# Optimization experiments

Measured on AMD Instinct MI355X. Metric: run time of the kernel, lower is better.

The kernel has to match this reference:

```python
import jax, jax.numpy as jnp
import numpy as np

D_MODEL = 512
NUM_HEADS = 8
D_K = D_MODEL // NUM_HEADS
LN_EPS = 1e-5


def setup_inputs() -> dict:
    key = jax.random.key(0)
    ks = jax.random.split(key, 11)
    d = D_MODEL
    s = 1.0 / np.sqrt(d)
    return {
        "x": jax.random.normal(ks[0], (4, 2048, d), dtype=jnp.float32),
        "Wq": jax.random.uniform(ks[1], (d, d), jnp.float32, -s, s),
        "bq": jax.random.uniform(ks[2], (d,), jnp.float32, -s, s),
        "Wk": jax.random.uniform(ks[3], (d, d), jnp.float32, -s, s),
        "bk": jax.random.uniform(ks[4], (d,), jnp.float32, -s, s),
        "Wv": jax.random.uniform(ks[5], (d, d), jnp.float32, -s, s),
        "bv": jax.random.uniform(ks[6], (d,), jnp.float32, -s, s),
        "Wo": jax.random.uniform(ks[7], (d, d), jnp.float32, -s, s),
        "bo": jax.random.uniform(ks[8], (d,), jnp.float32, -s, s),
        "gamma": jnp.ones((d,), jnp.float32),
        "beta": jnp.zeros((d,), jnp.float32),
    }


def reference(x, Wq, bq, Wk, bk, Wv, bv, Wo, bo, gamma, beta):
    # x: (B, S, D). Dropout is identity (eval mode).
    B, S, D = x.shape
    H, dk = NUM_HEADS, D_K
    # Linear layers use torch convention: y = x @ W.T + b
    q = (x @ Wq.T + bq).reshape(B, S, H, dk).transpose(0, 2, 1, 3)  # (B,H,S,dk)
    k = (x @ Wk.T + bk).reshape(B, S, H, dk).transpose(0, 2, 1, 3)
    v = (x @ Wv.T + bv).reshape(B, S, H, dk).transpose(0, 2, 1, 3)
    scores = jnp.einsum("bhqd,bhkd->bhqk", q, k) / jnp.sqrt(jnp.float32(dk))
    attn = jax.nn.softmax(scores, axis=-1)
    ctx = jnp.einsum("bhqk,bhkd->bhqd", attn, v)  # (B,H,S,dk)
    ctx = ctx.transpose(0, 2, 1, 3).reshape(B, S, D)
    out = ctx @ Wo.T + bo
    # residual + LayerNorm
    y = x + out
    mu = jnp.mean(y, axis=-1, keepdims=True)
    var = jnp.mean(jnp.square(y - mu), axis=-1, keepdims=True)
    return (y - mu) / jnp.sqrt(var + LN_EPS) * gamma + beta
```

## Files before the change

kernel.cpp:

```cpp
#include <hip/hip_runtime.h>
#include <math.h>

#define D 512
#define NH 8
#define DK 64
#define S 2048
#define BATCH 4
#define N_TOK (BATCH * S)

#define QSCALE 0.18033688f

typedef __bf16 bf16x8 __attribute__((ext_vector_type(8)));
typedef __bf16 bf16x4 __attribute__((ext_vector_type(4)));
typedef float f32x4 __attribute__((ext_vector_type(4)));

#define AS1 __attribute__((address_space(1)))
#define AS3 __attribute__((address_space(3)))

#define OFF_XB   0
#define OFF_WB   8388608
#define OFF_Q    10485760
#define OFF_K    18874368
#define OFF_VT   27262976
#define OFF_CTX  35651584
#define OFF_Y    10485760
#define OFF_FLAG 44040192

static __device__ __forceinline__ bf16x8 ldg8(const __bf16* p) {
    return *(const bf16x8*)p;
}
static __device__ __forceinline__ f32x4 mfma16(bf16x8 a, bf16x8 b, f32x4 c) {
    return __builtin_amdgcn_mfma_f32_16x16x32_bf16(a, b, c, 0, 0, 0);
}
static __device__ __forceinline__ float ldf(const void* p, size_t i, int isf) {
    return isf ? ((const float*)p)[i] : (float)(((const __bf16*)p)[i]);
}
static __device__ __forceinline__ float fexp2(float x) {
#if __has_builtin(__builtin_amdgcn_exp2f)
    return __builtin_amdgcn_exp2f(x);
#else
    return exp2f(x);
#endif
}
static __device__ __forceinline__ unsigned pack_trunc(float e0, float e1) {
    return (__builtin_bit_cast(unsigned, e0) >> 16)
         | (__builtin_bit_cast(unsigned, e1) & 0xFFFF0000u);
}
static __device__ __forceinline__ void gload_lds16(const void* g, void* l) {
    __builtin_amdgcn_global_load_lds((const AS1 char*)g, (AS3 char*)l, 16, 0, 0);
}

__global__ __launch_bounds__(256)
void cvt_kernel(const void* __restrict__ x,  const void* __restrict__ Wq,
                const void* __restrict__ Wk, const void* __restrict__ Wv,
                const void* __restrict__ Wo, __bf16* __restrict__ xb,
                __bf16* __restrict__ Wb, int* __restrict__ flag)
{
    const bf16x8 probe = ldg8((const __bf16*)x + (threadIdx.x & 63) * 8);
    int bad = 0;
#pragma unroll
    for (int j = 0; j < 8; ++j) bad |= !(fabsf((float)probe[j]) <= 64.0f);
    const int isf = __any(bad) ? 1 : 0;
    if (blockIdx.x == 0 && threadIdx.x == 0) *flag = isf;

    const size_t i0 = ((size_t)blockIdx.x * 256 + threadIdx.x) * 8;
    const void* src;
    __bf16* dst;
    size_t off;
    if (i0 < 4194304) {
        src = x; off = i0; dst = xb + i0;
    } else {
        const size_t wrel = i0 - 4194304;
        const size_t w = wrel >> 18;
        src = (w == 0) ? Wq : (w == 1) ? Wk : (w == 2) ? Wv : Wo;
        off = wrel & 262143;
        dst = Wb + wrel;
    }
    bf16x8 r;
    if (isf) {
        const float* f = (const float*)src + off;
#pragma unroll
        for (int j = 0; j < 8; ++j) r[j] = (__bf16)f[j];
    } else {
        r = *(const bf16x8*)((const __bf16*)src + off);
    }
    *(bf16x8*)dst = r;
}

__global__ __launch_bounds__(256)
void qkv_kernel(const __bf16* __restrict__ xb, const __bf16* __restrict__ Wb,
                const void* __restrict__ bq, const void* __restrict__ bk,
                const void* __restrict__ bv, const int* __restrict__ flag,
                __bf16* __restrict__ Q, __bf16* __restrict__ K,
                __bf16* __restrict__ Vt)
{
    __shared__ __align__(16) char smem[32768];

    const int isf = *flag;
    const int tid = threadIdx.x;
    const int w = tid >> 6, l = tid & 63;
    const int lane16 = l & 15, quad = l >> 4;
    const int wm = w >> 1, wn = w & 1;
    const int m0 = blockIdx.x * 128;
    const int by = blockIdx.y;
    const int n0 = by * 128;

    const int cwl = w * 64 + l;
    const int g0 = (cwl & 3) ^ ((cwl >> 3) & 3);
    const __bf16* aS0 = xb + (size_t)(m0 + (cwl >> 2)) * D + g0 * 8;
    const __bf16* aS1 = aS0 + (size_t)64 * D;
    const __bf16* bS0 = Wb + (size_t)(n0 + (cwl >> 2)) * D + g0 * 8;
    const __bf16* bS1 = bS0 + (size_t)64 * D;

    const int sw = (quad ^ ((lane16 >> 1) & 3)) * 16;
    const int aoff = (wm * 64 + lane16) * 64 + sw;
    const int boff = 8192 + (wn * 64 + lane16) * 64 + sw;

    f32x4 acc[4][4];
#pragma unroll
    for (int i = 0; i < 4; ++i)
#pragma unroll
        for (int j = 0; j < 4; ++j) acc[i][j] = (f32x4){0,0,0,0};

    gload_lds16(aS0, smem + w * 1024);
    gload_lds16(aS1, smem + 4096 + w * 1024);
    gload_lds16(bS0, smem + 8192 + w * 1024);
    gload_lds16(bS1, smem + 12288 + w * 1024);

    for (int kt = 0; kt < D / 32; ++kt) {
        __syncthreads();

        const char* bufp = smem + (kt & 1) * 16384;
        if (kt + 1 < D / 32) {
            char* nb = smem + ((kt + 1) & 1) * 16384;
            gload_lds16(aS0 + (kt + 1) * 32, nb + w * 1024);
            gload_lds16(aS1 + (kt + 1) * 32, nb + 4096 + w * 1024);
            gload_lds16(bS0 + (kt + 1) * 32, nb + 8192 + w * 1024);
            gload_lds16(bS1 + (kt + 1) * 32, nb + 12288 + w * 1024);
        }

        bf16x8 af[4], bf[4];
#pragma unroll
        for (int i = 0; i < 4; ++i) af[i] = *(const bf16x8*)(bufp + aoff + i * 1024);
#pragma unroll
        for (int j = 0; j < 4; ++j) bf[j] = *(const bf16x8*)(bufp + boff + j * 1024);
#pragma unroll
        for (int i = 0; i < 4; ++i)
#pragma unroll
            for (int j = 0; j < 4; ++j)
                acc[i][j] = mfma16(af[i], bf[j], acc[i][j]);
    }

    const int which = by >> 2;
    const int h = (by * 2 + wn) & 7;
    const float qs = (which == 0) ? QSCALE : 1.0f;
    const void* bias = (which == 0) ? bq : (which == 1) ? bk : bv;
    float bvv[4];
#pragma unroll
    for (int j = 0; j < 4; ++j)
        bvv[j] = ldf(bias, ((by & 3) * 128 + wn * 64 + 16 * j + lane16) & 511, isf);

    const int bb = m0 >> 11;
    const int ssb = (m0 & (S - 1)) + wm * 64;

    if (which < 2) {
        __bf16* out = ((which == 0) ? Q : K) + ((size_t)(bb * NH + h) * S) * DK;
#pragma unroll
        for (int i = 0; i < 4; ++i)
#pragma unroll
            for (int r = 0; r < 4; ++r) {
                const int ss = ssb + i * 16 + quad * 4 + r;
#pragma unroll
                for (int j = 0; j < 4; ++j)
                    out[(size_t)ss * DK + 16 * j + lane16] =
                        (__bf16)((acc[i][j][r] + bvv[j]) * qs);
            }
    } else {
#pragma unroll
        for (int i = 0; i < 4; ++i)
#pragma unroll
            for (int j = 0; j < 4; ++j) {
                const int dkc = 16 * j + lane16;
                __bf16* vp = Vt + ((size_t)(bb * NH + h) * DK + dkc) * S
                                + ssb + i * 16 + quad * 4;
                bf16x4 pkt;
#pragma unroll
                for (int r = 0; r < 4; ++r) pkt[r] = (__bf16)(acc[i][j][r] + bvv[j]);
                *(bf16x4*)vp = pkt;
            }
    }
}

__global__ __launch_bounds__(256)
void attn_kernel(const __bf16* __restrict__ Q, const __bf16* __restrict__ K,
                 const __bf16* __restrict__ Vt, __bf16* __restrict__ ctx)
{
    __shared__ __align__(16) char smem[49152];

    const int tid = threadIdx.x;
    const int w = tid >> 6, l = tid & 63;
    const int lane16 = l & 15, quad = l >> 4;

    const int lin = blockIdx.x;
    const int xcd = lin & 7;
    const int t = lin >> 3;
    const int bh = xcd * 4 + (t >> 4);
    const int qt = t & 15;
    const int b = bh >> 3, h = bh & 7;
    const size_t bhS = (size_t)bh * S;

    const int cwl = w * 64 + l;
    const char* kS[2];
    const char* vS[2];
#pragma unroll
    for (int c = 0; c < 2; ++c) {
        const int s = c * 256 + cwl;
        const int row = s >> 3;
        const int g = (s & 7) ^ (row & 7);
        kS[c] = (const char*)(K + (bhS + row) * DK) + g * 16;
        vS[c] = (const char*)(Vt + ((size_t)bh * DK + row) * S) + g * 16;
    }

    const int qbase = qt * 128 + w * 32;
    bf16x8 qa[2][2];
#pragma unroll
    for (int u = 0; u < 2; ++u) {
        const __bf16* Qp = Q + (bhS + qbase + u * 16 + lane16) * DK + quad * 8;
        qa[u][0] = ldg8(Qp);
        qa[u][1] = ldg8(Qp + 32);
    }

    bf16x8 aones;
#pragma unroll
    for (int j = 0; j < 8; ++j) aones[j] = (__bf16)1.0f;

    const int x7 = lane16 & 7;
    char* pw = smem + 32768 + w * 4096;
    const int pwoff = lane16 * 128 + ((quad & 1) * 8);
    const int proff = lane16 * 128;

    f32x4 o[2][4], lacc[2];
#pragma unroll
    for (int u = 0; u < 2; ++u) {
        lacc[u] = (f32x4){0,0,0,0};
#pragma unroll
        for (int tt = 0; tt < 4; ++tt) o[u][tt] = (f32x4){0,0,0,0};
    }

    gload_lds16(kS[0], smem + w * 1024);
    gload_lds16(kS[1], smem + 4096 + w * 1024);
    gload_lds16(vS[0], smem + 8192 + w * 1024);
    gload_lds16(vS[1], smem + 12288 + w * 1024);

    for (int kc = 0; kc < S / 64; ++kc) {
        __syncthreads();

        const int buf = kc & 1;
        const char* kb = smem + buf * 16384;
        const char* vb = kb + 8192;

        if (kc + 1 < S / 64) {
            char* kb2 = smem + (buf ^ 1) * 16384;
            gload_lds16(kS[0] + (size_t)(kc + 1) * 8192, kb2 + w * 1024);
            gload_lds16(kS[1] + (size_t)(kc + 1) * 8192, kb2 + 4096 + w * 1024);
            gload_lds16(vS[0] + (size_t)(kc + 1) * 128, kb2 + 8192 + w * 1024);
            gload_lds16(vS[1] + (size_t)(kc + 1) * 128, kb2 + 12288 + w * 1024);
        }

        bf16x8 kfA[4], kfB[4];
#pragma unroll
        for (int tt = 0; tt < 4; ++tt) {
            const int base = (tt * 16 + lane16) * 128;
            kfA[tt] = *(const bf16x8*)(kb + base + ((quad ^ x7) * 16));
            kfB[tt] = *(const bf16x8*)(kb + base + (((quad + 4) ^ x7) * 16));
        }

#pragma unroll
        for (int u = 0; u < 2; ++u) {
            f32x4 st[4];
#pragma unroll
            for (int tt = 0; tt < 4; ++tt) {
                f32x4 z = {0,0,0,0};
                z = mfma16(kfA[tt], qa[u][0], z);
                st[tt] = mfma16(kfB[tt], qa[u][1], z);
            }
#pragma unroll
            for (int tt = 0; tt < 4; ++tt) {
                uint2 pkt;
                pkt.x = pack_trunc(fexp2(st[tt][0]), fexp2(st[tt][1]));
                pkt.y = pack_trunc(fexp2(st[tt][2]), fexp2(st[tt][3]));
                *(uint2*)(pw + u * 2048 + pwoff
                          + (((tt * 2 + (quad >> 1)) ^ x7) * 16)) = pkt;
            }
        }

        bf16x8 vA[4], vB[4];
#pragma unroll
        for (int tt = 0; tt < 4; ++tt) {
            const int base = (tt * 16 + lane16) * 128;
            vA[tt] = *(const bf16x8*)(vb + base + ((quad ^ x7) * 16));
            vB[tt] = *(const bf16x8*)(vb + base + (((quad + 4) ^ x7) * 16));
        }
#pragma unroll
        for (int u = 0; u < 2; ++u) {
            const bf16x8 bp0 = *(const bf16x8*)(pw + u * 2048 + proff
                                                + (((0 + quad) ^ x7) * 16));
            const bf16x8 bp1 = *(const bf16x8*)(pw + u * 2048 + proff
                                                + (((4 + quad) ^ x7) * 16));
            lacc[u] = mfma16(aones, bp0, lacc[u]);
            lacc[u] = mfma16(aones, bp1, lacc[u]);
#pragma unroll
            for (int tt = 0; tt < 4; ++tt) {
                o[u][tt] = mfma16(vA[tt], bp0, o[u][tt]);
                o[u][tt] = mfma16(vB[tt], bp1, o[u][tt]);
            }
        }
    }

#pragma unroll
    for (int u = 0; u < 2; ++u) {
        const float inv = 1.0f / lacc[u][0];
        __bf16* cp = ctx + ((size_t)(b * S + qbase + u * 16 + lane16)) * D
                     + h * DK;
#pragma unroll
        for (int tt = 0; tt < 4; ++tt) {
            bf16x4 pkt;
#pragma unroll
            for (int r = 0; r < 4; ++r) pkt[r] = (__bf16)(o[u][tt][r] * inv);
            *(bf16x4*)(cp + tt * 16 + quad * 4) = pkt;
        }
    }
}

__global__ __launch_bounds__(256)
void proj_kernel(const __bf16* __restrict__ ctx, const __bf16* __restrict__ Wb,
                 const void* __restrict__ bo, const __bf16* __restrict__ xb,
                 const int* __restrict__ flag, __bf16* __restrict__ y)
{
    __shared__ __align__(16) char smem[24576];

    const int isf = *flag;
    const int tid = threadIdx.x;
    const int w = tid >> 6, l = tid & 63;
    const int lane16 = l & 15, quad = l >> 4;
    const int wm = w >> 1, wn = w & 1;
    const int m0 = blockIdx.x * 64;
    const int n0 = blockIdx.y * 128;

    const __bf16* Wo = Wb + (size_t)3 * 262144;
    const int cwl = w * 64 + l;
    const int g0 = (cwl & 3) ^ ((cwl >> 3) & 3);
    const __bf16* aS = ctx + (size_t)(m0 + (cwl >> 2)) * D + g0 * 8;
    const __bf16* bS0 = Wo + (size_t)(n0 + (cwl >> 2)) * D + g0 * 8;
    const __bf16* bS1 = bS0 + (size_t)64 * D;

    const int sw = (quad ^ ((lane16 >> 1) & 3)) * 16;
    const int aoff = (wm * 32 + lane16) * 64 + sw;
    const int boff = 4096 + (wn * 64 + lane16) * 64 + sw;

    f32x4 acc[2][4];
#pragma unroll
    for (int i = 0; i < 2; ++i)
#pragma unroll
        for (int j = 0; j < 4; ++j) acc[i][j] = (f32x4){0,0,0,0};

    gload_lds16(aS, smem + w * 1024);
    gload_lds16(bS0, smem + 4096 + w * 1024);
    gload_lds16(bS1, smem + 8192 + w * 1024);

    for (int kt = 0; kt < D / 32; ++kt) {
        __syncthreads();

        const char* bufp = smem + (kt & 1) * 12288;
        if (kt + 1 < D / 32) {
            char* nb = smem + ((kt + 1) & 1) * 12288;
            gload_lds16(aS + (kt + 1) * 32, nb + w * 1024);
            gload_lds16(bS0 + (kt + 1) * 32, nb + 4096 + w * 1024);
            gload_lds16(bS1 + (kt + 1) * 32, nb + 8192 + w * 1024);
        }

        bf16x8 af[2], bf[4];
#pragma unroll
        for (int i = 0; i < 2; ++i) af[i] = *(const bf16x8*)(bufp + aoff + i * 1024);
#pragma unroll
        for (int j = 0; j < 4; ++j) bf[j] = *(const bf16x8*)(bufp + boff + j * 1024);
#pragma unroll
        for (int i = 0; i < 2; ++i)
#pragma unroll
            for (int j = 0; j < 4; ++j)
                acc[i][j] = mfma16(af[i], bf[j], acc[i][j]);
    }

    float bvv[4];
#pragma unroll
    for (int j = 0; j < 4; ++j)
        bvv[j] = ldf(bo, n0 + wn * 64 + 16 * j + lane16, isf);

#pragma unroll
    for (int i = 0; i < 2; ++i)
#pragma unroll
        for (int r = 0; r < 4; ++r) {
            const int tok = m0 + wm * 32 + i * 16 + quad * 4 + r;
#pragma unroll
            for (int j = 0; j < 4; ++j) {
                const size_t idx = (size_t)tok * D + n0 + wn * 64 + 16 * j + lane16;
                y[idx] = (__bf16)(acc[i][j][r] + bvv[j] + (float)xb[idx]);
            }
        }
}

__global__ __launch_bounds__(256)
void ln_kernel(const __bf16* __restrict__ y, const void* __restrict__ gamma,
               const void* __restrict__ beta, const int* __restrict__ flag,
               void* __restrict__ out)
{
    const int isf = *flag;
    const int l = threadIdx.x & 63;
    const int tok = blockIdx.x * 4 + (threadIdx.x >> 6);
    const bf16x8 vv = ldg8(y + (size_t)tok * D + l * 8);

    float v[8];
    float sum = 0.f, sq = 0.f;
#pragma unroll
    for (int j = 0; j < 8; ++j) {
        v[j] = (float)vv[j];
        sum += v[j];
        sq  += v[j] * v[j];
    }
#pragma unroll
    for (int msk = 1; msk < 64; msk <<= 1) {
        sum += __shfl_xor(sum, msk);
        sq  += __shfl_xor(sq,  msk);
    }
    const float mean = sum * (1.0f / D);
    const float var  = sq * (1.0f / D) - mean * mean;
    const float rstd = rsqrtf(var + 1e-5f);

    const size_t base = (size_t)tok * D + l * 8;
#pragma unroll
    for (int j = 0; j < 8; ++j) {
        const float g  = ldf(gamma, l * 8 + j, isf);
        const float be = ldf(beta,  l * 8 + j, isf);
        const float r  = ((v[j] - mean) * rstd) * g + be;
        if (isf) ((float*)out)[base + j] = r;
        else     ((__bf16*)out)[base + j] = (__bf16)r;
    }
}

extern "C" void kernel_launch(void* const* d_in, const int* in_sizes, int n_in,
                              void* d_out, int out_size, void* d_ws,
                              size_t ws_size, hipStream_t stream)
{
    const void* x     = d_in[0];
    const void* Wq    = d_in[1];
    const void* bq    = d_in[2];
    const void* Wk    = d_in[3];
    const void* bk    = d_in[4];
    const void* Wv    = d_in[5];
    const void* bv    = d_in[6];
    const void* Wo    = d_in[7];
    const void* bo    = d_in[8];
    const void* gamma = d_in[9];
    const void* beta  = d_in[10];

    char* ws = (char*)d_ws;
    __bf16* xb  = (__bf16*)(ws + OFF_XB);
    __bf16* Wb  = (__bf16*)(ws + OFF_WB);
    __bf16* Qb  = (__bf16*)(ws + OFF_Q);
    __bf16* Kb  = (__bf16*)(ws + OFF_K);
    __bf16* Vtb = (__bf16*)(ws + OFF_VT);
    __bf16* ctx = (__bf16*)(ws + OFF_CTX);
    __bf16* y   = (__bf16*)(ws + OFF_Y);
    int*    flag = (int*)(ws + OFF_FLAG);

    cvt_kernel<<<5242880 / (256 * 8), 256, 0, stream>>>(
        x, Wq, Wk, Wv, Wo, xb, Wb, flag);
    qkv_kernel<<<dim3(N_TOK / 128, 12), 256, 0, stream>>>(
        xb, Wb, bq, bk, bv, flag, Qb, Kb, Vtb);
    attn_kernel<<<dim3(512), 256, 0, stream>>>(Qb, Kb, Vtb, ctx);
    proj_kernel<<<dim3(N_TOK / 64, 4), 256, 0, stream>>>(
        ctx, Wb, bo, xb, flag, y);
    ln_kernel<<<dim3(N_TOK / 4), 256, 0, stream>>>(y, gamma, beta, flag, d_out);
}
```

Before: 190.5 us.

## Split attention block across 8 waves with 16 query rows each

The attention kernel now launches 512 threads per block instead of 256, and each of the 8 waves handles 16 query rows instead of 32. Each thread loads one K and one V segment per tile instead of two, and the per-wave P scratch shrinks to 2 KB. The goal is to cut per-thread register use and raise the number of waves hiding latency. The cost is that each K/V fragment read from LDS is reused for fewer queries, so LDS traffic per MFMA doubles.

```diff
diff --git a/kernel.cpp b/kernel.cpp
--- a/kernel.cpp
+++ b/kernel.cpp
@@ -191,7 +191,7 @@
     }
 }
 
-__global__ __launch_bounds__(256)
+__global__ __launch_bounds__(512, 4)
 void attn_kernel(const __bf16* __restrict__ Q, const __bf16* __restrict__ K,
                  const __bf16* __restrict__ Vt, __bf16* __restrict__ ctx)
 {
@@ -210,24 +210,17 @@
     const size_t bhS = (size_t)bh * S;
 
     const int cwl = w * 64 + l;
-    const char* kS[2];
-    const char* vS[2];
-#pragma unroll
-    for (int c = 0; c < 2; ++c) {
-        const int s = c * 256 + cwl;
-        const int row = s >> 3;
-        const int g = (s & 7) ^ (row & 7);
-        kS[c] = (const char*)(K + (bhS + row) * DK) + g * 16;
-        vS[c] = (const char*)(Vt + ((size_t)bh * DK + row) * S) + g * 16;
-    }
-
-    const int qbase = qt * 128 + w * 32;
-    bf16x8 qa[2][2];
-#pragma unroll
-    for (int u = 0; u < 2; ++u) {
-        const __bf16* Qp = Q + (bhS + qbase + u * 16 + lane16) * DK + quad * 8;
-        qa[u][0] = ldg8(Qp);
-        qa[u][1] = ldg8(Qp + 32);
+    const int row = cwl >> 3;
+    const int g = (cwl & 7) ^ (row & 7);
+    const char* kS = (const char*)(K + (bhS + row) * DK) + g * 16;
+    const char* vS = (const char*)(Vt + ((size_t)bh * DK + row) * S) + g * 16;
+
+    const int qbase = qt * 128 + w * 16;
+    bf16x8 qa0, qa1;
+    {
+        const __bf16* Qp = Q + (bhS + qbase + lane16) * DK + quad * 8;
+        qa0 = ldg8(Qp);
+        qa1 = ldg8(Qp + 32);
     }
 
     bf16x8 aones;
@@ -235,22 +228,17 @@
     for (int j = 0; j < 8; ++j) aones[j] = (__bf16)1.0f;
 
     const int x7 = lane16 & 7;
-    char* pw = smem + 32768 + w * 4096;
+    char* pw = smem + 32768 + w * 2048;
     const int pwoff = lane16 * 128 + ((quad & 1) * 8);
     const int proff = lane16 * 128;
 
-    f32x4 o[2][4], lacc[2];
-#pragma unroll
-    for (int u = 0; u < 2; ++u) {
-        lacc[u] = (f32x4){0,0,0,0};
-#pragma unroll
-        for (int tt = 0; tt < 4; ++tt) o[u][tt] = (f32x4){0,0,0,0};
-    }
-
-    gload_lds16(kS[0], smem + w * 1024);
-    gload_lds16(kS[1], smem + 4096 + w * 1024);
-    gload_lds16(vS[0], smem + 8192 + w * 1024);
-    gload_lds16(vS[1], smem + 12288 + w * 1024);
+    f32x4 o[4], lacc;
+    lacc = (f32x4){0,0,0,0};
+#pragma unroll
+    for (int tt = 0; tt < 4; ++tt) o[tt] = (f32x4){0,0,0,0};
+
+    gload_lds16(kS, smem + w * 1024);
+    gload_lds16(vS, smem + 8192 + w * 1024);
 
     for (int kc = 0; kc < S / 64; ++kc) {
         __syncthreads();
@@ -261,10 +249,8 @@
 
         if (kc + 1 < S / 64) {
             char* kb2 = smem + (buf ^ 1) * 16384;
-            gload_lds16(kS[0] + (size_t)(kc + 1) * 8192, kb2 + w * 1024);
-            gload_lds16(kS[1] + (size_t)(kc + 1) * 8192, kb2 + 4096 + w * 1024);
-            gload_lds16(vS[0] + (size_t)(kc + 1) * 128, kb2 + 8192 + w * 1024);
-            gload_lds16(vS[1] + (size_t)(kc + 1) * 128, kb2 + 12288 + w * 1024);
+            gload_lds16(kS + (size_t)(kc + 1) * 8192, kb2 + w * 1024);
+            gload_lds16(vS + (size_t)(kc + 1) * 128, kb2 + 8192 + w * 1024);
         }
 
         bf16x8 kfA[4], kfB[4];
@@ -275,21 +261,20 @@
             kfB[tt] = *(const bf16x8*)(kb + base + (((quad + 4) ^ x7) * 16));
         }
 
-#pragma unroll
-        for (int u = 0; u < 2; ++u) {
+        {
             f32x4 st[4];
 #pragma unroll
             for (int tt = 0; tt < 4; ++tt) {
                 f32x4 z = {0,0,0,0};
-                z = mfma16(kfA[tt], qa[u][0], z);
-                st[tt] = mfma16(kfB[tt], qa[u][1], z);
+                z = mfma16(kfA[tt], qa0, z);
+                st[tt] = mfma16(kfB[tt], qa1, z);
             }
 #pragma unroll
             for (int tt = 0; tt < 4; ++tt) {
                 uint2 pkt;
                 pkt.x = pack_trunc(fexp2(st[tt][0]), fexp2(st[tt][1]));
                 pkt.y = pack_trunc(fexp2(st[tt][2]), fexp2(st[tt][3]));
-                *(uint2*)(pw + u * 2048 + pwoff
+                *(uint2*)(pw + pwoff
                           + (((tt * 2 + (quad >> 1)) ^ x7) * 16)) = pkt;
             }
         }
@@ -301,32 +286,29 @@
             vA[tt] = *(const bf16x8*)(vb + base + ((quad ^ x7) * 16));
             vB[tt] = *(const bf16x8*)(vb + base + (((quad + 4) ^ x7) * 16));
         }
-#pragma unroll
-        for (int u = 0; u < 2; ++u) {
-            const bf16x8 bp0 = *(const bf16x8*)(pw + u * 2048 + proff
+        {
+            const bf16x8 bp0 = *(const bf16x8*)(pw + proff
                                                 + (((0 + quad) ^ x7) * 16));
-            const bf16x8 bp1 = *(const bf16x8*)(pw + u * 2048 + proff
+            const bf16x8 bp1 = *(const bf16x8*)(pw + proff
                                                 + (((4 + quad) ^ x7) * 16));
-            lacc[u] = mfma16(aones, bp0, lacc[u]);
-            lacc[u] = mfma16(aones, bp1, lacc[u]);
+            lacc = mfma16(aones, bp0, lacc);
+            lacc = mfma16(aones, bp1, lacc);
 #pragma unroll
             for (int tt = 0; tt < 4; ++tt) {
-                o[u][tt] = mfma16(vA[tt], bp0, o[u][tt]);
-                o[u][tt] = mfma16(vB[tt], bp1, o[u][tt]);
-            }
-        }
-    }
-
-#pragma unroll
-    for (int u = 0; u < 2; ++u) {
-        const float inv = 1.0f / lacc[u][0];
-        __bf16* cp = ctx + ((size_t)(b * S + qbase + u * 16 + lane16)) * D
-                     + h * DK;
+                o[tt] = mfma16(vA[tt], bp0, o[tt]);
+                o[tt] = mfma16(vB[tt], bp1, o[tt]);
+            }
+        }
+    }
+
+    {
+        const float inv = 1.0f / lacc[0];
+        __bf16* cp = ctx + ((size_t)(b * S + qbase + lane16)) * D + h * DK;
 #pragma unroll
         for (int tt = 0; tt < 4; ++tt) {
             bf16x4 pkt;
 #pragma unroll
-            for (int r = 0; r < 4; ++r) pkt[r] = (__bf16)(o[u][tt][r] * inv);
+            for (int r = 0; r < 4; ++r) pkt[r] = (__bf16)(o[tt][r] * inv);
             *(bf16x4*)(cp + tt * 16 + quad * 4) = pkt;
         }
     }
@@ -477,7 +459,7 @@
         x, Wq, Wk, Wv, Wo, xb, Wb, flag);
     qkv_kernel<<<dim3(N_TOK / 128, 12), 256, 0, stream>>>(
         xb, Wb, bq, bk, bv, flag, Qb, Kb, Vtb);
-    attn_kernel<<<dim3(512), 256, 0, stream>>>(Qb, Kb, Vtb, ctx);
+    attn_kernel<<<dim3(512), 512, 0, stream>>>(Qb, Kb, Vtb, ctx);
     proj_kernel<<<dim3(N_TOK / 64, 4), 256, 0, stream>>>(
         ctx, Wb, bo, xb, flag, y);
     ln_kernel<<<dim3(N_TOK / 4), 256, 0, stream>>>(y, gamma, beta, flag, d_out);
```

After: 183.1 us. 1.04x faster.

## Split attention key range across two wave teams and keep P in registers

Applied to the files above, without the earlier changes.

The attention kernel now runs 512 threads in two teams of four waves. Each team processes alternate 64-key chunks for the same 128 queries, and the partial outputs and row sums are merged through LDS at the end. Probabilities are packed straight into MFMA B-operand registers instead of being round-tripped through shared memory, and the V-transpose store layout in the QKV kernel is permuted to match this register layout. The aim is more waves per query tile and no LDS traffic for P, at the cost of 64KB of LDS per block, a final reduction step and possible occupancy limits.

```diff
diff --git a/kernel.cpp b/kernel.cpp
--- a/kernel.cpp
+++ b/kernel.cpp
@@ -13,6 +13,7 @@
 typedef __bf16 bf16x8 __attribute__((ext_vector_type(8)));
 typedef __bf16 bf16x4 __attribute__((ext_vector_type(4)));
 typedef float f32x4 __attribute__((ext_vector_type(4)));
+typedef unsigned int u32x4 __attribute__((ext_vector_type(4)));
 
 #define AS1 __attribute__((address_space(1)))
 #define AS3 __attribute__((address_space(3)))
@@ -182,7 +183,7 @@
             for (int j = 0; j < 4; ++j) {
                 const int dkc = 16 * j + lane16;
                 __bf16* vp = Vt + ((size_t)(bb * NH + h) * DK + dkc) * S
-                                + ssb + i * 16 + quad * 4;
+                                + ssb + (quad + 4 * (i >> 1)) * 8 + 4 * (i & 1);
                 bf16x4 pkt;
 #pragma unroll
                 for (int r = 0; r < 4; ++r) pkt[r] = (__bf16)(acc[i][j][r] + bvv[j]);
@@ -191,15 +192,16 @@
     }
 }
 
-__global__ __launch_bounds__(256)
+__global__ __launch_bounds__(512, 4)
 void attn_kernel(const __bf16* __restrict__ Q, const __bf16* __restrict__ K,
                  const __bf16* __restrict__ Vt, __bf16* __restrict__ ctx)
 {
-    __shared__ __align__(16) char smem[49152];
+    __shared__ __align__(16) char smem[65536];
 
     const int tid = threadIdx.x;
     const int w = tid >> 6, l = tid & 63;
     const int lane16 = l & 15, quad = l >> 4;
+    const int team = w >> 2, tq = w & 3;
 
     const int lin = blockIdx.x;
     const int xcd = lin & 7;
@@ -210,18 +212,12 @@
     const size_t bhS = (size_t)bh * S;
 
     const int cwl = w * 64 + l;
-    const char* kS[2];
-    const char* vS[2];
-#pragma unroll
-    for (int c = 0; c < 2; ++c) {
-        const int s = c * 256 + cwl;
-        const int row = s >> 3;
-        const int g = (s & 7) ^ (row & 7);
-        kS[c] = (const char*)(K + (bhS + row) * DK) + g * 16;
-        vS[c] = (const char*)(Vt + ((size_t)bh * DK + row) * S) + g * 16;
-    }
-
-    const int qbase = qt * 128 + w * 32;
+    const int row = cwl >> 3;
+    const int g = (cwl & 7) ^ (row & 7);
+    const char* kS = (const char*)(K + (bhS + row) * DK) + g * 16;
+    const char* vS = (const char*)(Vt + ((size_t)bh * DK + row) * S) + g * 16;
+
+    const int qbase = qt * 128 + tq * 32;
     bf16x8 qa[2][2];
 #pragma unroll
     for (int u = 0; u < 2; ++u) {
@@ -235,9 +231,6 @@
     for (int j = 0; j < 8; ++j) aones[j] = (__bf16)1.0f;
 
     const int x7 = lane16 & 7;
-    char* pw = smem + 32768 + w * 4096;
-    const int pwoff = lane16 * 128 + ((quad & 1) * 8);
-    const int proff = lane16 * 128;
 
     f32x4 o[2][4], lacc[2];
 #pragma unroll
@@ -247,87 +240,109 @@
         for (int tt = 0; tt < 4; ++tt) o[u][tt] = (f32x4){0,0,0,0};
     }
 
-    gload_lds16(kS[0], smem + w * 1024);
-    gload_lds16(kS[1], smem + 4096 + w * 1024);
-    gload_lds16(vS[0], smem + 8192 + w * 1024);
-    gload_lds16(vS[1], smem + 12288 + w * 1024);
-
-    for (int kc = 0; kc < S / 64; ++kc) {
+    gload_lds16(kS, smem + w * 1024);
+    gload_lds16(vS, smem + 8192 + w * 1024);
+    gload_lds16(kS + 8192, smem + 32768 + w * 1024);
+    gload_lds16(vS + 128, smem + 32768 + 8192 + w * 1024);
+
+    for (int p = 0; p < S / 128; ++p) {
         __syncthreads();
 
-        const int buf = kc & 1;
-        const char* kb = smem + buf * 16384;
+        const char* kb = smem + (team * 2 + (p & 1)) * 16384;
         const char* vb = kb + 8192;
 
-        if (kc + 1 < S / 64) {
-            char* kb2 = smem + (buf ^ 1) * 16384;
-            gload_lds16(kS[0] + (size_t)(kc + 1) * 8192, kb2 + w * 1024);
-            gload_lds16(kS[1] + (size_t)(kc + 1) * 8192, kb2 + 4096 + w * 1024);
-            gload_lds16(vS[0] + (size_t)(kc + 1) * 128, kb2 + 8192 + w * 1024);
-            gload_lds16(vS[1] + (size_t)(kc + 1) * 128, kb2 + 12288 + w * 1024);
-        }
-
-        bf16x8 kfA[4], kfB[4];
+        if (p + 1 < S / 128) {
+            const int ns = (p + 1) & 1;
+            const size_t c1 = 2 * p + 2, c2 = 2 * p + 3;
+            char* b1 = smem + ns * 16384;
+            char* b2 = smem + (2 + ns) * 16384;
+            gload_lds16(kS + c1 * 8192, b1 + w * 1024);
+            gload_lds16(vS + c1 * 128,  b1 + 8192 + w * 1024);
+            gload_lds16(kS + c2 * 8192, b2 + w * 1024);
+            gload_lds16(vS + c2 * 128,  b2 + 8192 + w * 1024);
+        }
+
+        f32x4 st[2][4];
 #pragma unroll
         for (int tt = 0; tt < 4; ++tt) {
             const int base = (tt * 16 + lane16) * 128;
-            kfA[tt] = *(const bf16x8*)(kb + base + ((quad ^ x7) * 16));
-            kfB[tt] = *(const bf16x8*)(kb + base + (((quad + 4) ^ x7) * 16));
-        }
-
+            const bf16x8 kfA = *(const bf16x8*)(kb + base + ((quad ^ x7) * 16));
+            const bf16x8 kfB = *(const bf16x8*)(kb + base
+                                                + (((quad + 4) ^ x7) * 16));
+#pragma unroll
+            for (int u = 0; u < 2; ++u) {
+                f32x4 z = {0,0,0,0};
+                z = mfma16(kfA, qa[u][0], z);
+                st[u][tt] = mfma16(kfB, qa[u][1], z);
+            }
+        }
+
+        bf16x8 bp[2][2];
 #pragma unroll
         for (int u = 0; u < 2; ++u) {
-            f32x4 st[4];
-#pragma unroll
-            for (int tt = 0; tt < 4; ++tt) {
-                f32x4 z = {0,0,0,0};
-                z = mfma16(kfA[tt], qa[u][0], z);
-                st[tt] = mfma16(kfB[tt], qa[u][1], z);
-            }
-#pragma unroll
-            for (int tt = 0; tt < 4; ++tt) {
-                uint2 pkt;
-                pkt.x = pack_trunc(fexp2(st[tt][0]), fexp2(st[tt][1]));
-                pkt.y = pack_trunc(fexp2(st[tt][2]), fexp2(st[tt][3]));
-                *(uint2*)(pw + u * 2048 + pwoff
-                          + (((tt * 2 + (quad >> 1)) ^ x7) * 16)) = pkt;
-            }
-        }
-
-        bf16x8 vA[4], vB[4];
+            u32x4 u0, u1;
+            u0[0] = pack_trunc(fexp2(st[u][0][0]), fexp2(st[u][0][1]));
+            u0[1] = pack_trunc(fexp2(st[u][0][2]), fexp2(st[u][0][3]));
+            u0[2] = pack_trunc(fexp2(st[u][1][0]), fexp2(st[u][1][1]));
+            u0[3] = pack_trunc(fexp2(st[u][1][2]), fexp2(st[u][1][3]));
+            u1[0] = pack_trunc(fexp2(st[u][2][0]), fexp2(st[u][2][1]));
+            u1[1] = pack_trunc(fexp2(st[u][2][2]), fexp2(st[u][2][3]));
+            u1[2] = pack_trunc(fexp2(st[u][3][0]), fexp2(st[u][3][1]));
+            u1[3] = pack_trunc(fexp2(st[u][3][2]), fexp2(st[u][3][3]));
+            bp[u][0] = __builtin_bit_cast(bf16x8, u0);
+            bp[u][1] = __builtin_bit_cast(bf16x8, u1);
+        }
+
 #pragma unroll
         for (int tt = 0; tt < 4; ++tt) {
             const int base = (tt * 16 + lane16) * 128;
-            vA[tt] = *(const bf16x8*)(vb + base + ((quad ^ x7) * 16));
-            vB[tt] = *(const bf16x8*)(vb + base + (((quad + 4) ^ x7) * 16));
+            const bf16x8 vA = *(const bf16x8*)(vb + base + ((quad ^ x7) * 16));
+            const bf16x8 vB = *(const bf16x8*)(vb + base
+                                               + (((quad + 4) ^ x7) * 16));
+#pragma unroll
+            for (int u = 0; u < 2; ++u) {
+                o[u][tt] = mfma16(vA, bp[u][0], o[u][tt]);
+                o[u][tt] = mfma16(vB, bp[u][1], o[u][tt]);
+            }
         }
 #pragma unroll
         for (int u = 0; u < 2; ++u) {
-            const bf16x8 bp0 = *(const bf16x8*)(pw + u * 2048 + proff
-                                                + (((0 + quad) ^ x7) * 16));
-            const bf16x8 bp1 = *(const bf16x8*)(pw + u * 2048 + proff
-                                                + (((4 + quad) ^ x7) * 16));
-            lacc[u] = mfma16(aones, bp0, lacc[u]);
-            lacc[u] = mfma16(aones, bp1, lacc[u]);
+            lacc[u] = mfma16(aones, bp[u][0], lacc[u]);
+            lacc[u] = mfma16(aones, bp[u][1], lacc[u]);
+        }
+    }
+
+    __syncthreads();
+    if (team == 1) {
+        char* obase = smem + tq * 8192;
+#pragma unroll
+        for (int u = 0; u < 2; ++u)
+#pragma unroll
+            for (int tt = 0; tt < 4; ++tt)
+                *(f32x4*)(obase + (u * 4 + tt) * 1024 + l * 16) = o[u][tt];
+        float* lb = (float*)(smem + 32768 + tq * 512 + l * 8);
+        lb[0] = lacc[0][0];
+        lb[1] = lacc[1][0];
+    }
+    __syncthreads();
+    if (team == 0) {
+        const char* obase = smem + tq * 8192;
+        const float* lb = (const float*)(smem + 32768 + tq * 512 + l * 8);
+#pragma unroll
+        for (int u = 0; u < 2; ++u) {
+            const float inv = 1.0f / (lacc[u][0] + lb[u]);
+            __bf16* cp = ctx + ((size_t)(b * S + qbase + u * 16 + lane16)) * D
+                         + h * DK;
 #pragma unroll
             for (int tt = 0; tt < 4; ++tt) {
-                o[u][tt] = mfma16(vA[tt], bp0, o[u][tt]);
-                o[u][tt] = mfma16(vB[tt], bp1, o[u][tt]);
-            }
-        }
-    }
-
-#pragma unroll
-    for (int u = 0; u < 2; ++u) {
-        const float inv = 1.0f / lacc[u][0];
-        __bf16* cp = ctx + ((size_t)(b * S + qbase + u * 16 + lane16)) * D
-                     + h * DK;
-#pragma unroll
-        for (int tt = 0; tt < 4; ++tt) {
-            bf16x4 pkt;
-#pragma unroll
-            for (int r = 0; r < 4; ++r) pkt[r] = (__bf16)(o[u][tt][r] * inv);
-            *(bf16x4*)(cp + tt * 16 + quad * 4) = pkt;
+                const f32x4 po = *(const f32x4*)(obase + (u * 4 + tt) * 1024
+                                                 + l * 16);
+                bf16x4 pkt;
+#pragma unroll
+                for (int r = 0; r < 4; ++r)
+                    pkt[r] = (__bf16)((o[u][tt][r] + po[r]) * inv);
+                *(bf16x4*)(cp + tt * 16 + quad * 4) = pkt;
+            }
         }
     }
 }
@@ -477,7 +492,7 @@
         x, Wq, Wk, Wv, Wo, xb, Wb, flag);
     qkv_kernel<<<dim3(N_TOK / 128, 12), 256, 0, stream>>>(
         xb, Wb, bq, bk, bv, flag, Qb, Kb, Vtb);
-    attn_kernel<<<dim3(512), 256, 0, stream>>>(Qb, Kb, Vtb, ctx);
+    attn_kernel<<<dim3(512), 512, 0, stream>>>(Qb, Kb, Vtb, ctx);
     proj_kernel<<<dim3(N_TOK / 64, 4), 256, 0, stream>>>(
         ctx, Wb, bo, xb, flag, y);
     ln_kernel<<<dim3(N_TOK / 4), 256, 0, stream>>>(y, gamma, beta, flag, d_out);
```

After: 174.8 us. 1.09x faster.
